# Optimization experiments

Measured on AMD Instinct MI355X. Metric: run time of the kernel, lower is better.

The kernel has to match this reference:

```python
import jax, jax.numpy as jnp
import numpy as np
from math import factorial

L_MAX = 8
N_POINTS = 1_000_000


def _make_F(l_max):
    n = (l_max + 1) * (l_max + 2) // 2
    F = np.empty((n,), dtype=np.float64)
    for l in range(l_max + 1):
        for m in range(l + 1):
            F[l * (l + 1) // 2 + m] = (-1) ** m * np.sqrt(
                (2 * l + 1) / (2 * np.pi) * factorial(l - m) / factorial(l + m)
            )
    return jnp.asarray(F, dtype=jnp.float32)


def setup_inputs() -> dict:
    key = jax.random.key(0)
    xyz = jax.random.normal(key, (N_POINTS, 3), dtype=jnp.float32)
    F = _make_F(L_MAX)
    return {"xyz": xyz, "F": F}


def reference(xyz, F):
    l_max = L_MAX
    # normalize to unit sphere
    rsq = jnp.sum(xyz ** 2, axis=1)
    u = xyz / jnp.sqrt(rsq)[:, None]
    x, y, z = u[:, 0], u[:, 1], u[:, 2]

    # associated-Legendre-like recurrence (same math/signs as the torch module)
    Q = {(0, 0): jnp.ones_like(x)}
    for l in range(1, l_max + 1):
        Q[(l, l)] = -(2 * l - 1) * Q[(l - 1, l - 1)]
        Q[(l, l - 1)] = -z * Q[(l, l)]
        for m in range(0, l - 1):
            Q[(l, m)] = ((2 * l - 1) * z * Q[(l - 1, m)] - (l + m - 1) * Q[(l - 2, m)]) / (l - m)

    # trig recurrence: s_m = Im[(x+iy)^m], c_m = Re[(x+iy)^m]
    s = [jnp.zeros_like(x)]
    c = [jnp.ones_like(x)]
    for m in range(1, l_max + 1):
        s.append(x * s[m - 1] + y * c[m - 1])
        c.append(x * c[m - 1] - y * s[m - 1])

    inv_sqrt2 = 1.0 / np.sqrt(2.0)
    cols = []  # ordered as Y[:, l*l + l + m]
    for l in range(l_max + 1):
        base = l * (l + 1) // 2
        for m in range(-l, 0):
            cols.append(F[base - m] * Q[(l, -m)] * s[-m])
        cols.append(F[base] * Q[(l, 0)] * inv_sqrt2)
        for m in range(1, l + 1):
            cols.append(F[base + m] * Q[(l, m)] * c[m])
    return jnp.stack(cols, axis=1)  # [N, (l_max+1)^2]
```

## Files before the change

### kernel.cpp

```cpp
#include <hip/hip_runtime.h>

constexpr int LMAX = 8;
constexpr int NCOL = (LMAX + 1) * (LMAX + 1);
constexpr int PTS  = 64;
constexpr int TILE_FLOATS = PTS * NCOL;
constexpr int VEC4_ITERS  = TILE_FLOATS / 4 / PTS;

__device__ __forceinline__ void emit_col(float* row, const float* __restrict__ F,
                                         int l, int m, float Q, float sm, float cm) {
    const int fbase = l * (l + 1) / 2;
    const int cbase = l * l + l;
    if (m == 0) {
        const float inv_sqrt2 = 0.70710678118654752440f;
        row[cbase] = F[fbase] * Q * inv_sqrt2;
    } else {
        float t = F[fbase + m] * Q;
        row[cbase - m] = t * sm;
        row[cbase + m] = t * cm;
    }
}

__global__ __launch_bounds__(PTS) void sh_kernel(const float* __restrict__ xyz,
                                                 const float* __restrict__ F,
                                                 float* __restrict__ out, int n) {
    __shared__ float tile[TILE_FLOATS];
    const int lane    = threadIdx.x;
    const int base_pt = blockIdx.x * PTS;
    const int i       = base_pt + lane;

    float x = 0.0f, y = 0.0f, z = 1.0f;
    if (i < n) {
        x = xyz[3 * i + 0];
        y = xyz[3 * i + 1];
        z = xyz[3 * i + 2];
    }
    const float rsq  = x * x + y * y + z * z;
    const float rinv = rsqrtf(rsq);
    x *= rinv; y *= rinv; z *= rinv;

    float* row = &tile[lane * NCOL];

    float Qmm = 1.0f;
    float sm = 0.0f, cm = 1.0f;

#pragma unroll
    for (int m = 0; m <= LMAX; ++m) {
        if (m > 0) {
            Qmm = -(float)(2 * m - 1) * Qmm;
            const float s_new = x * sm + y * cm;
            const float c_new = x * cm - y * sm;
            sm = s_new; cm = c_new;
        }
        float Qp = Qmm;
        emit_col(row, F, m, m, Qp, sm, cm);
        if (m < LMAX) {
            float Qc = (float)(2 * m + 1) * z * Qmm;
            emit_col(row, F, m + 1, m, Qc, sm, cm);
#pragma unroll
            for (int l = m + 2; l <= LMAX; ++l) {
                const float Qn = ((float)(2 * l - 1) * z * Qc
                                  - (float)(l + m - 1) * Qp) * (1.0f / (float)(l - m));
                Qp = Qc; Qc = Qn;
                emit_col(row, F, l, m, Qc, sm, cm);
            }
        }
    }

    __syncthreads();

    const long long tile_base = (long long)base_pt * NCOL;
    if (base_pt + PTS <= n) {
        const float4* src = (const float4*)tile;
        float4* dst = (float4*)(out + tile_base);
#pragma unroll
        for (int k = 0; k < VEC4_ITERS; ++k) {
            dst[k * PTS + lane] = src[k * PTS + lane];
        }
        out[tile_base + VEC4_ITERS * PTS * 4 + lane] = tile[VEC4_ITERS * PTS * 4 + lane];
    } else {
        const long long lim = (long long)n * NCOL;
        for (int k = lane; k < TILE_FLOATS; k += PTS) {
            const long long gi = tile_base + k;
            if (gi < lim) out[gi] = tile[k];
        }
    }
}

extern "C" void kernel_launch(void* const* d_in, const int* in_sizes, int n_in,
                              void* d_out, int out_size, void* d_ws, size_t ws_size,
                              hipStream_t stream) {
    const float* xyz = (const float*)d_in[0];
    const float* F   = (const float*)d_in[1];
    float* out       = (float*)d_out;
    const int n      = in_sizes[0] / 3;
    const int grid   = (n + PTS - 1) / PTS;
    sh_kernel<<<grid, PTS, 0, stream>>>(xyz, F, out, n);
}
```

Baseline: 334.4 us.

## Split each point's harmonics across two threads by m parity

Each block now handles 32 points with 64 threads. One half of the threads computes even-m columns and the other half odd-m columns, stepping the trig and Q_mm recurrences by two. The aim is to shorten each thread's serial recurrence chain and cut register pressure, with a launch-bounds hint for occupancy. On a 64-wide wavefront the two halves diverge within the same wave, so the split may serialize rather than parallelize.

Measured after the change: 331.4 us. Within noise of the previous version (-0.9%).

```diff
diff --git a/kernel.cpp b/kernel.cpp
--- a/kernel.cpp
+++ b/kernel.cpp
@@ -2,9 +2,10 @@
 
 constexpr int LMAX = 8;
 constexpr int NCOL = (LMAX + 1) * (LMAX + 1);
-constexpr int PTS  = 64;
-constexpr int TILE_FLOATS = PTS * NCOL;
-constexpr int VEC4_ITERS  = TILE_FLOATS / 4 / PTS;
+constexpr int PPB  = 32;
+constexpr int THREADS = 64;
+constexpr int TILE_FLOATS = PPB * NCOL;
+constexpr int TILE_VEC4   = TILE_FLOATS / 4;
 
 __device__ __forceinline__ void emit_col(float* row, const float* __restrict__ F,
                                          int l, int m, float Q, float sm, float cm) {
@@ -20,36 +21,21 @@
     }
 }
 
-__global__ __launch_bounds__(PTS) void sh_kernel(const float* __restrict__ xyz,
-                                                 const float* __restrict__ F,
-                                                 float* __restrict__ out, int n) {
-    __shared__ float tile[TILE_FLOATS];
-    const int lane    = threadIdx.x;
-    const int base_pt = blockIdx.x * PTS;
-    const int i       = base_pt + lane;
-
-    float x = 0.0f, y = 0.0f, z = 1.0f;
-    if (i < n) {
-        x = xyz[3 * i + 0];
-        y = xyz[3 * i + 1];
-        z = xyz[3 * i + 2];
-    }
-    const float rsq  = x * x + y * y + z * z;
-    const float rinv = rsqrtf(rsq);
-    x *= rinv; y *= rinv; z *= rinv;
-
-    float* row = &tile[lane * NCOL];
-
-    float Qmm = 1.0f;
-    float sm = 0.0f, cm = 1.0f;
+template <int M0>
+__device__ __forceinline__ void compute_half(float* row, const float* __restrict__ F,
+                                             float x, float y, float z) {
+    float sm, cm, Qmm;
+    if (M0 == 0) { sm = 0.0f; cm = 1.0f; Qmm = 1.0f; }
+    else         { sm = y;    cm = x;    Qmm = -1.0f; }
 
 #pragma unroll
-    for (int m = 0; m <= LMAX; ++m) {
-        if (m > 0) {
-            Qmm = -(float)(2 * m - 1) * Qmm;
-            const float s_new = x * sm + y * cm;
-            const float c_new = x * cm - y * sm;
-            sm = s_new; cm = c_new;
+    for (int m = M0; m <= LMAX; m += 2) {
+        if (m > M0) {
+            const float s1 = x * sm + y * cm;
+            const float c1 = x * cm - y * sm;
+            sm = x * s1 + y * c1;
+            cm = x * c1 - y * s1;
+            Qmm *= (float)((2 * m - 1) * (2 * m - 3));
         }
         float Qp = Qmm;
         emit_col(row, F, m, m, Qp, sm, cm);
@@ -65,21 +51,49 @@
             }
         }
     }
+}
+
+__global__ __launch_bounds__(THREADS, 4) void sh_kernel(const float* __restrict__ xyz,
+                                                        const float* __restrict__ F,
+                                                        float* __restrict__ out, int n) {
+    __shared__ float tile[TILE_FLOATS];
+    const int lane    = threadIdx.x;
+    const int p       = lane & 31;
+    const int half    = lane >> 5;
+    const int base_pt = blockIdx.x * PPB;
+    const int i       = base_pt + p;
+
+    float x = 0.0f, y = 0.0f, z = 1.0f;
+    if (i < n) {
+        x = xyz[3 * i + 0];
+        y = xyz[3 * i + 1];
+        z = xyz[3 * i + 2];
+    }
+    const float rsq  = x * x + y * y + z * z;
+    const float rinv = rsqrtf(rsq);
+    x *= rinv; y *= rinv; z *= rinv;
+
+    float* row = &tile[p * NCOL];
+
+    if (half == 0) compute_half<0>(row, F, x, y, z);
+    else           compute_half<1>(row, F, x, y, z);
 
     __syncthreads();
 
     const long long tile_base = (long long)base_pt * NCOL;
-    if (base_pt + PTS <= n) {
+    if (base_pt + PPB <= n) {
         const float4* src = (const float4*)tile;
         float4* dst = (float4*)(out + tile_base);
 #pragma unroll
-        for (int k = 0; k < VEC4_ITERS; ++k) {
-            dst[k * PTS + lane] = src[k * PTS + lane];
+        for (int k = 0; k < 10; ++k) {
+            dst[k * THREADS + lane] = src[k * THREADS + lane];
         }
-        out[tile_base + VEC4_ITERS * PTS * 4 + lane] = tile[VEC4_ITERS * PTS * 4 + lane];
+        if (lane < TILE_VEC4 - 10 * THREADS) {
+            dst[10 * THREADS + lane] = src[10 * THREADS + lane];
+        }
     } else {
         const long long lim = (long long)n * NCOL;
-        for (int k = lane; k < TILE_FLOATS; k += PTS) {
+        for (int k = lane; k < TILE_FLOATS; k += THREADS) {
             const long long gi = tile_base + k;
             if (gi < lim) out[gi] = tile[k];
         }
@@ -93,6 +107,6 @@
     const float* F   = (const float*)d_in[1];
     float* out       = (float*)d_out;
     const int n      = in_sizes[0] / 3;
-    const int grid   = (n + PTS - 1) / PTS;
-    sh_kernel<<<grid, PTS, 0, stream>>>(xyz, F, out, n);
+    const int grid   = (n + PPB - 1) / PPB;
+    sh_kernel<<<grid, THREADS, 0, stream>>>(xyz, F, out, n);
 }
```
